# Kernel optimization log

Hardware: AMD Instinct MI355X
Metric: run time of the kernel (lower is better)

The kernel has to match this reference:

```python
import jax, jax.numpy as jnp
import numpy as np

N_NODES = 100000
NEG_SLOPE = 0.01


def setup_inputs() -> dict:
    key = jax.random.key(0)
    k1, k2, k3, k4 = jax.random.split(key, 4)
    E = 1600000
    x = jax.random.normal(k1, (N_NODES, 256), dtype=jnp.float32)
    edge_index = jax.random.randint(k2, (2, E), 0, N_NODES, dtype=jnp.int64)
    # Glorot-ish init for GCN linear weights
    W1 = jax.random.normal(k3, (256, 128), dtype=jnp.float32) / np.sqrt(256.0)
    b1 = jnp.zeros((128,), dtype=jnp.float32)
    W2 = jax.random.normal(k4, (128, 64), dtype=jnp.float32) / np.sqrt(128.0)
    b2 = jnp.zeros((64,), dtype=jnp.float32)
    return {"x": x, "edge_index": edge_index, "W1": W1, "b1": b1, "W2": W2, "b2": b2}


def _gcn_norm(edge_index, n_nodes):
    # Add self-loops (PyG GCNConv default), symmetric normalization.
    loops = jnp.arange(n_nodes, dtype=edge_index.dtype)
    src = jnp.concatenate([edge_index[0], loops])
    dst = jnp.concatenate([edge_index[1], loops])
    deg = jax.ops.segment_sum(jnp.ones_like(dst, dtype=jnp.float32), dst,
                              num_segments=n_nodes)
    dinv = jnp.where(deg > 0, 1.0 / jnp.sqrt(deg), 0.0)
    norm = dinv[src] * dinv[dst]  # [E + N]
    return src, dst, norm


def _gcn_conv(h, W, b, src, dst, norm, n_nodes):
    h = h @ W                              # [N, out] linear transform first
    msg = h[src] * norm[:, None]           # gather + edge weighting
    agg = jax.ops.segment_sum(msg, dst, num_segments=n_nodes)  # scatter-add
    return agg + b


def reference(x, edge_index, W1, b1, W2, b2):
    n = x.shape[0]
    src, dst, norm = _gcn_norm(edge_index, n)
    h = _gcn_conv(x, W1, b1, src, dst, norm, n)
    h = jnp.where(h >= 0, h, NEG_SLOPE * h)  # leaky_relu, slope 0.01
    return _gcn_conv(h, W2, b2, src, dst, norm, n)
```

## Files before the change

### kernel.cpp

```cpp
#include <hip/hip_runtime.h>
#include <hip/hip_bf16.h>
#include <stdint.h>

#define GPART 512
#define BSHIFT 9
#define BSIZE 512
#define MAXNB 512

typedef short short8 __attribute__((ext_vector_type(8)));
typedef float f32x4 __attribute__((ext_vector_type(4)));
union U4S8 { uint4 u; short8 s; };

static __device__ __forceinline__ float bflo(uint32_t h){ return __uint_as_float(h << 16); }
static __device__ __forceinline__ float bfhi(uint32_t h){ return __uint_as_float(h & 0xFFFF0000u); }
static __device__ __forceinline__ uint32_t f2bf_bits(float f){
  uint32_t u = __float_as_uint(f);
  return (u + 0x7FFFu + ((u >> 16) & 1u)) >> 16;
}
static __device__ __forceinline__ uint32_t pack2bf(float lo, float hi){
  return f2bf_bits(lo) | (f2bf_bits(hi) << 16);
}

__global__ __launch_bounds__(256) void k_hist(const int* __restrict__ dst, int E, int NB,
    int* __restrict__ gHist){
  __shared__ int lh[MAXNB];
  int blk = blockIdx.x;
  for (int i = threadIdx.x; i < NB; i += 256) lh[i] = 0;
  __syncthreads();
  int chunk = (E + GPART - 1) / GPART;
  int e0 = blk * chunk, e1 = min(E, e0 + chunk);
  for (int e = e0 + threadIdx.x; e < e1; e += 256)
    atomicAdd(&lh[dst[e] >> BSHIFT], 1);
  __syncthreads();
  for (int i = threadIdx.x; i < NB; i += 256) gHist[i * GPART + blk] = lh[i];
}

__global__ __launch_bounds__(64) void k_scanA(int* __restrict__ gHist,
    int* __restrict__ bucketTotal){
  int b = blockIdx.x;
  int lane = threadIdx.x;
  int carry = 0;
  #pragma unroll
  for (int r = 0; r < GPART/64; ++r){
    int v = gHist[b*GPART + r*64 + lane];
    int pref = v;
    #pragma unroll
    for (int off = 1; off < 64; off <<= 1){ int t = __shfl_up(pref, off); if (lane >= off) pref += t; }
    int tot = __shfl(pref, 63);
    gHist[b*GPART + r*64 + lane] = carry + pref - v;
    carry += tot;
  }
  if (lane == 0) bucketTotal[b] = carry;
}

__global__ __launch_bounds__(64) void k_scanB(const int* __restrict__ bucketTotal, int NB,
    int* __restrict__ bucketBase){
  int lane = threadIdx.x;
  int carry = 0;
  for (int r = 0; r*64 < NB; ++r){
    int idx = r*64 + lane;
    int v = (idx < NB) ? bucketTotal[idx] : 0;
    int pref = v;
    #pragma unroll
    for (int off = 1; off < 64; off <<= 1){ int t = __shfl_up(pref, off); if (lane >= off) pref += t; }
    int tot = __shfl(pref, 63);
    if (idx < NB) bucketBase[idx] = carry + pref - v;
    carry += tot;
  }
}

__global__ __launch_bounds__(256) void k_scatter(const int* __restrict__ src,
    const int* __restrict__ dst, int E, int NB,
    const int* __restrict__ gHist, const int* __restrict__ bucketBase,
    uint32_t* __restrict__ edgesP){
  __shared__ int lpos[MAXNB];
  int blk = blockIdx.x;
  for (int i = threadIdx.x; i < NB; i += 256) lpos[i] = 0;
  __syncthreads();
  int chunk = (E + GPART - 1) / GPART;
  int e0 = blk * chunk, e1 = min(E, e0 + chunk);
  for (int e = e0 + threadIdx.x; e < e1; e += 256){
    int s = src[e], d = dst[e];
    int b = d >> BSHIFT;
    int o = atomicAdd(&lpos[b], 1);
    int pos = bucketBase[b] + gHist[b*GPART + blk] + o;
    edgesP[pos] = (uint32_t)s | ((uint32_t)(d & (BSIZE-1)) << 23);
  }
}

__global__ __launch_bounds__(256) void k_csr_p1(const uint32_t* __restrict__ edgesP,
    const int* __restrict__ bucketBase, const int* __restrict__ bucketTotal,
    int n, int* __restrict__ start, int* __restrict__ cnt, float* __restrict__ dinv){
  __shared__ int cnt_l[BSIZE], start_l[BSIZE];
  int b = blockIdx.x;
  int base = bucketBase[b], total = bucketTotal[b];
  int d0 = b << BSHIFT;
  int tid = threadIdx.x;
  for (int i = tid; i < BSIZE; i += 256) cnt_l[i] = 0;
  __syncthreads();
  for (int i = tid; i < total; i += 256)
    atomicAdd(&cnt_l[edgesP[base + i] >> 23], 1);
  __syncthreads();
  if (tid < 64){
    int lane = tid, carry = 0;
    #pragma unroll
    for (int r = 0; r < BSIZE/64; ++r){
      int v = cnt_l[r*64 + lane];
      int pref = v;
      #pragma unroll
      for (int off = 1; off < 64; off <<= 1){ int t = __shfl_up(pref, off); if (lane >= off) pref += t; }
      int tot = __shfl(pref, 63);
      start_l[r*64 + lane] = carry + pref - v;
      carry += tot;
    }
  }
  __syncthreads();
  for (int i = tid; i < BSIZE; i += 256){
    int d = d0 + i;
    if (d < n){
      int c = cnt_l[i];
      cnt[d] = c;
      start[d] = base + start_l[i];
      dinv[d] = rsqrtf((float)(c + 1));
    }
  }
}

__global__ __launch_bounds__(256) void k_csr_p2(const uint32_t* __restrict__ edgesP,
    const int* __restrict__ bucketBase, const int* __restrict__ bucketTotal,
    const int* __restrict__ start, const float* __restrict__ dinv,
    int2* __restrict__ csr){
  __shared__ int fp[BSIZE];
  int b = blockIdx.x;
  int base = bucketBase[b], total = bucketTotal[b];
  int d0 = b << BSHIFT;
  int tid = threadIdx.x;
  for (int i = tid; i < BSIZE; i += 256) fp[i] = 0;
  __syncthreads();
  for (int i = tid; i < total; i += 256){
    uint32_t w = edgesP[base + i];
    int dl = (int)(w >> 23);
    int s = (int)(w & 0x7FFFFFu);
    int p = atomicAdd(&fp[dl], 1);
    float wt = dinv[s] * dinv[d0 + dl];
    csr[start[d0 + dl] + p] = make_int2(s, __float_as_int(wt));
  }
}

__global__ __launch_bounds__(256) void k_packW(const float* __restrict__ W,
    uint4* __restrict__ Wf, int K, int Nc){
  int s = blockIdx.x * 256 + threadIdx.x;
  int total = (K >> 5) * (Nc >> 4) * 64;
  if (s >= total) return;
  int lane = s & 63;
  int frag = s >> 6;
  int NT = Nc >> 4;
  int nt = frag % NT, ks = frag / NT;
  int col = nt*16 + (lane & 15);
  int k0  = ks*32 + (lane >> 4)*8;
  float v[8];
  #pragma unroll
  for (int e = 0; e < 8; ++e) v[e] = W[(size_t)(k0 + e)*Nc + col];
  uint4 u;
  u.x = pack2bf(v[0], v[1]); u.y = pack2bf(v[2], v[3]);
  u.z = pack2bf(v[4], v[5]); u.w = pack2bf(v[6], v[7]);
  Wf[s] = u;
}

__global__ __launch_bounds__(256) void k_gemm1_lds(const float* __restrict__ X,
    const uint4* __restrict__ W1f, unsigned short* __restrict__ H1, int n){
  __shared__ float xs[32][256];
  int tid = threadIdx.x;
  int wid = tid >> 6, lane = tid & 63;
  int row0 = blockIdx.x * 32;
  #pragma unroll
  for (int i = 0; i < 8; ++i){
    int r = wid*8 + i;
    int gr = min(row0 + r, n - 1);
    const float* gsrc = X + (size_t)gr*256 + 4*(lane ^ (r & 7));
    __builtin_amdgcn_global_load_lds(
        (const __attribute__((address_space(1))) unsigned int*)gsrc,
        (__attribute__((address_space(3))) unsigned int*)(&xs[r][0]),
        16, 0, 0);
  }
  __syncthreads();
  int mhalf = wid & 1, nh = wid >> 1;
  int rA = lane & 15, kg = lane >> 4;
  int lrow = mhalf*16 + rA;
  f32x4 acc[4];
  #pragma unroll
  for (int nt = 0; nt < 4; ++nt) acc[nt] = (f32x4){0.f, 0.f, 0.f, 0.f};
  #pragma unroll
  for (int ks = 0; ks < 8; ++ks){
    int g0 = ks*8 + kg*2;
    float4 f0 = *(const float4*)&xs[lrow][4*( g0      ^ (rA & 7))];
    float4 f1 = *(const float4*)&xs[lrow][4*((g0 + 1) ^ (rA & 7))];
    U4S8 a;
    a.u.x = pack2bf(f0.x, f0.y); a.u.y = pack2bf(f0.z, f0.w);
    a.u.z = pack2bf(f1.x, f1.y); a.u.w = pack2bf(f1.z, f1.w);
    #pragma unroll
    for (int nt = 0; nt < 4; ++nt){
      U4S8 b; b.u = W1f[(ks*8 + nh*4 + nt)*64 + lane];
      acc[nt] = __builtin_amdgcn_mfma_f32_16x16x32_bf16(a.s, b.s, acc[nt], 0, 0, 0);
    }
  }
  int rowbase = row0 + mhalf*16 + kg*4;
  #pragma unroll
  for (int r = 0; r < 4; ++r){
    int row = rowbase + r;
    if (row < n){
      #pragma unroll
      for (int nt = 0; nt < 4; ++nt)
        H1[(size_t)row*128 + (nh*4 + nt)*16 + rA] = (unsigned short)f2bf_bits(acc[nt][r]);
    }
  }
}

__global__ __launch_bounds__(256) void k_agg1(const uint4* __restrict__ H1,
    const int2* __restrict__ csr,
    const int* __restrict__ start, const int* __restrict__ cnt,
    const float* __restrict__ dinv, const float* __restrict__ b1,
    uint4* __restrict__ A1, int n){
  int w = (int)((blockIdx.x * blockDim.x + threadIdx.x) >> 6);
  int lane = threadIdx.x & 63;
  if (w >= n) return;
  int g = lane >> 4, li = lane & 15;
  float dw = dinv[w];
  float sw = (g == 0) ? dw * dw : 0.f;
  uint4 hs = H1[(size_t)w*16 + li];
  float acc[8];
  acc[0]=sw*bflo(hs.x); acc[1]=sw*bfhi(hs.x); acc[2]=sw*bflo(hs.y); acc[3]=sw*bfhi(hs.y);
  acc[4]=sw*bflo(hs.z); acc[5]=sw*bfhi(hs.z); acc[6]=sw*bflo(hs.w); acc[7]=sw*bfhi(hs.w);
  int e0 = start[w], deg = cnt[w];
  for (int base = 0; base < deg; base += 64){
    int nin = min(64, deg - base);
    int2 ew = (lane < nin) ? csr[e0 + base + lane] : make_int2(0, 0);
    for (int j = 0; j < nin; j += 8){
      int   sA = __shfl(ew.x, j + g);
      float wA = __uint_as_float((uint32_t)__shfl(ew.y, j + g));
      int   sB = __shfl(ew.x, j + 4 + g);
      float wB = __uint_as_float((uint32_t)__shfl(ew.y, j + 4 + g));
      uint4 hA = H1[(size_t)sA*16 + li];
      uint4 hB = H1[(size_t)sB*16 + li];
      acc[0]=fmaf(wA,bflo(hA.x),acc[0]); acc[1]=fmaf(wA,bfhi(hA.x),acc[1]);
      acc[2]=fmaf(wA,bflo(hA.y),acc[2]); acc[3]=fmaf(wA,bfhi(hA.y),acc[3]);
      acc[4]=fmaf(wA,bflo(hA.z),acc[4]); acc[5]=fmaf(wA,bfhi(hA.z),acc[5]);
      acc[6]=fmaf(wA,bflo(hA.w),acc[6]); acc[7]=fmaf(wA,bfhi(hA.w),acc[7]);
      acc[0]=fmaf(wB,bflo(hB.x),acc[0]); acc[1]=fmaf(wB,bfhi(hB.x),acc[1]);
      acc[2]=fmaf(wB,bflo(hB.y),acc[2]); acc[3]=fmaf(wB,bfhi(hB.y),acc[3]);
      acc[4]=fmaf(wB,bflo(hB.z),acc[4]); acc[5]=fmaf(wB,bfhi(hB.z),acc[5]);
      acc[6]=fmaf(wB,bflo(hB.w),acc[6]); acc[7]=fmaf(wB,bfhi(hB.w),acc[7]);
    }
  }
  #pragma unroll
  for (int e = 0; e < 8; ++e){
    acc[e] += __shfl_xor(acc[e], 16);
    acc[e] += __shfl_xor(acc[e], 32);
  }
  float4 bA = *(const float4*)&b1[li*8];
  float4 bB = *(const float4*)&b1[li*8 + 4];
  acc[0]+=bA.x; acc[1]+=bA.y; acc[2]+=bA.z; acc[3]+=bA.w;
  acc[4]+=bB.x; acc[5]+=bB.y; acc[6]+=bB.z; acc[7]+=bB.w;
  #pragma unroll
  for (int e = 0; e < 8; ++e) acc[e] = (acc[e] >= 0.f) ? acc[e] : 0.01f * acc[e];
  if (g == 0){
    uint4 o;
    o.x = pack2bf(acc[0], acc[1]); o.y = pack2bf(acc[2], acc[3]);
    o.z = pack2bf(acc[4], acc[5]); o.w = pack2bf(acc[6], acc[7]);
    A1[(size_t)w*16 + li] = o;
  }
}

__global__ __launch_bounds__(256) void k_gemm2_mfma(const uint4* __restrict__ A1,
    const uint4* __restrict__ W2f, unsigned short* __restrict__ H2, int n){
  int wv = (int)((blockIdx.x * 256u + threadIdx.x) >> 6);
  int lane = threadIdx.x & 63;
  int row0 = wv * 16;
  if (row0 >= n) return;
  int rA = lane & 15, kg = lane >> 4;
  f32x4 acc[4];
  #pragma unroll
  for (int nt = 0; nt < 4; ++nt) acc[nt] = (f32x4){0.f, 0.f, 0.f, 0.f};
  int r0 = min(row0 + rA, n - 1);
  const uint4* arow = A1 + (size_t)r0*16 + kg;
  uint4 u = arow[0];
  #pragma unroll
  for (int ks = 0; ks < 4; ++ks){
    U4S8 a; a.u = u;
    if (ks < 3) u = arow[(ks+1)*4];
    #pragma unroll
    for (int nt = 0; nt < 4; ++nt){
      U4S8 b; b.u = W2f[(ks*4 + nt)*64 + lane];
      acc[nt] = __builtin_amdgcn_mfma_f32_16x16x32_bf16(a.s, b.s, acc[nt], 0, 0, 0);
    }
  }
  #pragma unroll
  for (int r = 0; r < 4; ++r){
    int row = row0 + kg*4 + r;
    if (row < n){
      #pragma unroll
      for (int nt = 0; nt < 4; ++nt)
        H2[(size_t)row*64 + nt*16 + rA] = (unsigned short)f2bf_bits(acc[nt][r]);
    }
  }
}

__global__ __launch_bounds__(256) void k_agg2(const uint4* __restrict__ H2,
    const int2* __restrict__ csr,
    const int* __restrict__ start, const int* __restrict__ cnt,
    const float* __restrict__ dinv, const float* __restrict__ b2,
    float* __restrict__ out, int n){
  int w = (int)((blockIdx.x * blockDim.x + threadIdx.x) >> 6);
  int lane = threadIdx.x & 63;
  if (w >= n) return;
  int g = lane >> 3, li = lane & 7;
  float dw = dinv[w];
  float sw = (g == 0) ? dw * dw : 0.f;
  uint4 hs = H2[(size_t)w*8 + li];
  float acc[8];
  acc[0]=sw*bflo(hs.x); acc[1]=sw*bfhi(hs.x); acc[2]=sw*bflo(hs.y); acc[3]=sw*bfhi(hs.y);
  acc[4]=sw*bflo(hs.z); acc[5]=sw*bfhi(hs.z); acc[6]=sw*bflo(hs.w); acc[7]=sw*bfhi(hs.w);
  int e0 = start[w], deg = cnt[w];
  for (int base = 0; base < deg; base += 64){
    int nin = min(64, deg - base);
    int2 ew = (lane < nin) ? csr[e0 + base + lane] : make_int2(0, 0);
    for (int j = 0; j < nin; j += 16){
      int   sA = __shfl(ew.x, j + g);
      float wA = __uint_as_float((uint32_t)__shfl(ew.y, j + g));
      int   sB = __shfl(ew.x, j + 8 + g);
      float wB = __uint_as_float((uint32_t)__shfl(ew.y, j + 8 + g));
      uint4 hA = H2[(size_t)sA*8 + li];
      uint4 hB = H2[(size_t)sB*8 + li];
      acc[0]=fmaf(wA,bflo(hA.x),acc[0]); acc[1]=fmaf(wA,bfhi(hA.x),acc[1]);
      acc[2]=fmaf(wA,bflo(hA.y),acc[2]); acc[3]=fmaf(wA,bfhi(hA.y),acc[3]);
      acc[4]=fmaf(wA,bflo(hA.z),acc[4]); acc[5]=fmaf(wA,bfhi(hA.z),acc[5]);
      acc[6]=fmaf(wA,bflo(hA.w),acc[6]); acc[7]=fmaf(wA,bfhi(hA.w),acc[7]);
      acc[0]=fmaf(wB,bflo(hB.x),acc[0]); acc[1]=fmaf(wB,bfhi(hB.x),acc[1]);
      acc[2]=fmaf(wB,bflo(hB.y),acc[2]); acc[3]=fmaf(wB,bfhi(hB.y),acc[3]);
      acc[4]=fmaf(wB,bflo(hB.z),acc[4]); acc[5]=fmaf(wB,bfhi(hB.z),acc[5]);
      acc[6]=fmaf(wB,bflo(hB.w),acc[6]); acc[7]=fmaf(wB,bfhi(hB.w),acc[7]);
    }
  }
  #pragma unroll
  for (int e = 0; e < 8; ++e){
    acc[e] += __shfl_xor(acc[e], 8);
    acc[e] += __shfl_xor(acc[e], 16);
    acc[e] += __shfl_xor(acc[e], 32);
  }
  float4 bA = *(const float4*)&b2[li*8];
  float4 bB = *(const float4*)&b2[li*8 + 4];
  acc[0]+=bA.x; acc[1]+=bA.y; acc[2]+=bA.z; acc[3]+=bA.w;
  acc[4]+=bB.x; acc[5]+=bB.y; acc[6]+=bB.z; acc[7]+=bB.w;
  if (g == 0){
    float4 o0 = make_float4(acc[0], acc[1], acc[2], acc[3]);
    float4 o1 = make_float4(acc[4], acc[5], acc[6], acc[7]);
    *(float4*)&out[(size_t)w*64 + li*8]     = o0;
    *(float4*)&out[(size_t)w*64 + li*8 + 4] = o1;
  }
}

extern "C" void kernel_launch(void* const* d_in, const int* in_sizes, int n_in,
                              void* d_out, int out_size, void* d_ws, size_t ws_size,
                              hipStream_t stream){
  const float* x  = (const float*)d_in[0];
  const int*   ei = (const int*)d_in[1];
  const float* W1 = (const float*)d_in[2];
  const float* b1 = (const float*)d_in[3];
  const float* W2 = (const float*)d_in[4];
  const float* b2 = (const float*)d_in[5];
  float* out = (float*)d_out;

  int N = in_sizes[0] / 256;
  int E = in_sizes[1] / 2;
  int NB = (N + BSIZE - 1) >> BSHIFT;

  char* p = (char*)d_ws;
  uint32_t* H1   = (uint32_t*)p;  p += (size_t)N*64*4;
  uint32_t* A1   = (uint32_t*)p;  p += (size_t)N*64*4;
  uint32_t* H2   = (uint32_t*)p;  p += (size_t)N*32*4;
  uint32_t* edgesP=(uint32_t*)p;  p += (size_t)E*4;
  int2* csr      = (int2*)p;      p += (size_t)E*8;
  int* gHist     = (int*)p;       p += (size_t)NB*GPART*4;
  int* bucketTotal=(int*)p;       p += (size_t)((NB+63)&~63)*4;
  int* bucketBase= (int*)p;       p += (size_t)((NB+63)&~63)*4;
  uint4* W1f     = (uint4*)p;     p += 8*8*64*16;
  uint4* W2f     = (uint4*)p;     p += 4*4*64*16;
  int* start     = (int*)p;       p += (size_t)N*4;
  int* cnt       = (int*)p;       p += (size_t)N*4;
  float* dinv    = (float*)p;     p += (size_t)N*4;

  const int* srcIdx = ei;
  const int* dstIdx = ei + E;

  int nG1Blocks = (N + 31) / 32;
  int nW2 = (N + 15) / 16;
  int nG2Blocks = (nW2 + 3) / 4;
  int nNodeBlocks = (N + 3) / 4;

  k_packW<<<(8*8*64 + 255)/256, 256, 0, stream>>>(W1, W1f, 256, 128);
  k_packW<<<(4*4*64 + 255)/256, 256, 0, stream>>>(W2, W2f, 128, 64);
  k_hist<<<GPART, 256, 0, stream>>>(dstIdx, E, NB, gHist);
  k_scanA<<<NB, 64, 0, stream>>>(gHist, bucketTotal);
  k_scanB<<<1, 64, 0, stream>>>(bucketTotal, NB, bucketBase);
  k_scatter<<<GPART, 256, 0, stream>>>(srcIdx, dstIdx, E, NB, gHist, bucketBase, edgesP);
  k_csr_p1<<<NB, 256, 0, stream>>>(edgesP, bucketBase, bucketTotal, N, start, cnt, dinv);
  k_csr_p2<<<NB, 256, 0, stream>>>(edgesP, bucketBase, bucketTotal, start, dinv, csr);
  k_gemm1_lds<<<nG1Blocks, 256, 0, stream>>>(x, W1f, (unsigned short*)H1, N);
  k_agg1<<<nNodeBlocks, 256, 0, stream>>>((const uint4*)H1, csr, start, cnt, dinv, b1, (uint4*)A1, N);
  k_gemm2_mfma<<<nG2Blocks, 256, 0, stream>>>((const uint4*)A1, W2f, (unsigned short*)H2, N);
  k_agg2<<<nNodeBlocks, 256, 0, stream>>>((const uint4*)H2, csr, start, cnt, dinv, b2, out, N);
}
```

Baseline: 216.3 us.

## Split GEMM1 tiles across CSR-build kernels as extra blocks to overlap work

The standalone GEMM1 kernel is removed. Its 32-row tiles are distributed by fixed ratios across the histogram, scatter and two CSR-build kernels, which run as extra blocks alongside the graph-preprocessing blocks. This targets the idle CUs left by the small, latency-bound CSR kernels and drops one launch. In exchange every fused kernel reserves 32KB of shared memory, which can lower occupancy for the build blocks, and the split ratios are hand-tuned.

```diff
diff --git a/kernel.cpp b/kernel.cpp
--- a/kernel.cpp
+++ b/kernel.cpp
@@ -21,18 +21,75 @@
   return f2bf_bits(lo) | (f2bf_bits(hi) << 16);
 }
 
-__global__ __launch_bounds__(256) void k_hist(const int* __restrict__ dst, int E, int NB,
-    int* __restrict__ gHist){
-  __shared__ int lh[MAXNB];
+static __device__ __forceinline__ void gemm1_tile(const float* __restrict__ X,
+    const uint4* __restrict__ W1f, unsigned short* __restrict__ H1, int n,
+    int row0, char* smem, int tid){
+  float (*xs)[256] = (float (*)[256])smem;
+  int wid = tid >> 6, lane = tid & 63;
+  #pragma unroll
+  for (int i = 0; i < 8; ++i){
+    int r = wid*8 + i;
+    int gr = min(row0 + r, n - 1);
+    const float* gsrc = X + (size_t)gr*256 + 4*(lane ^ (r & 7));
+    __builtin_amdgcn_global_load_lds(
+        (const __attribute__((address_space(1))) unsigned int*)gsrc,
+        (__attribute__((address_space(3))) unsigned int*)(&xs[r][0]),
+        16, 0, 0);
+  }
+  __syncthreads();
+  int mhalf = wid & 1, nh = wid >> 1;
+  int rA = lane & 15, kg = lane >> 4;
+  int lrow = mhalf*16 + rA;
+  f32x4 acc[4];
+  #pragma unroll
+  for (int nt = 0; nt < 4; ++nt) acc[nt] = (f32x4){0.f, 0.f, 0.f, 0.f};
+  #pragma unroll
+  for (int ks = 0; ks < 8; ++ks){
+    int g0 = ks*8 + kg*2;
+    float4 f0 = *(const float4*)&xs[lrow][4*( g0      ^ (rA & 7))];
+    float4 f1 = *(const float4*)&xs[lrow][4*((g0 + 1) ^ (rA & 7))];
+    U4S8 a;
+    a.u.x = pack2bf(f0.x, f0.y); a.u.y = pack2bf(f0.z, f0.w);
+    a.u.z = pack2bf(f1.x, f1.y); a.u.w = pack2bf(f1.z, f1.w);
+    #pragma unroll
+    for (int nt = 0; nt < 4; ++nt){
+      U4S8 b; b.u = W1f[(ks*8 + nh*4 + nt)*64 + lane];
+      acc[nt] = __builtin_amdgcn_mfma_f32_16x16x32_bf16(a.s, b.s, acc[nt], 0, 0, 0);
+    }
+  }
+  int rowbase = row0 + mhalf*16 + kg*4;
+  #pragma unroll
+  for (int r = 0; r < 4; ++r){
+    int row = rowbase + r;
+    if (row < n){
+      #pragma unroll
+      for (int nt = 0; nt < 4; ++nt)
+        H1[(size_t)row*128 + (nh*4 + nt)*16 + rA] = (unsigned short)f2bf_bits(acc[nt][r]);
+    }
+  }
+}
+
+__global__ __launch_bounds__(256) void k_fat_hist(const int* __restrict__ dst, int E, int NB,
+    int* __restrict__ gHist,
+    const float* __restrict__ X, const uint4* __restrict__ W1f,
+    unsigned short* __restrict__ H1, int n, int g1base, int nbuild){
+  __shared__ __align__(16) char smem[32768];
+  int tid = threadIdx.x;
+  if ((int)blockIdx.x >= nbuild){
+    int row0 = (g1base + (int)blockIdx.x - nbuild) * 32;
+    gemm1_tile(X, W1f, H1, n, row0, smem, tid);
+    return;
+  }
+  int* lh = (int*)smem;
   int blk = blockIdx.x;
-  for (int i = threadIdx.x; i < NB; i += 256) lh[i] = 0;
+  for (int i = tid; i < NB; i += 256) lh[i] = 0;
   __syncthreads();
   int chunk = (E + GPART - 1) / GPART;
   int e0 = blk * chunk, e1 = min(E, e0 + chunk);
-  for (int e = e0 + threadIdx.x; e < e1; e += 256)
+  for (int e = e0 + tid; e < e1; e += 256)
     atomicAdd(&lh[dst[e] >> BSHIFT], 1);
   __syncthreads();
-  for (int i = threadIdx.x; i < NB; i += 256) gHist[i * GPART + blk] = lh[i];
+  for (int i = tid; i < NB; i += 256) gHist[i * GPART + blk] = lh[i];
 }
 
 __global__ __launch_bounds__(64) void k_scanA(int* __restrict__ gHist,
@@ -69,17 +126,26 @@
   }
 }
 
-__global__ __launch_bounds__(256) void k_scatter(const int* __restrict__ src,
+__global__ __launch_bounds__(256) void k_fat_scatter(const int* __restrict__ src,
     const int* __restrict__ dst, int E, int NB,
     const int* __restrict__ gHist, const int* __restrict__ bucketBase,
-    uint32_t* __restrict__ edgesP){
-  __shared__ int lpos[MAXNB];
+    uint32_t* __restrict__ edgesP,
+    const float* __restrict__ X, const uint4* __restrict__ W1f,
+    unsigned short* __restrict__ H1, int n, int g1base, int nbuild){
+  __shared__ __align__(16) char smem[32768];
+  int tid = threadIdx.x;
+  if ((int)blockIdx.x >= nbuild){
+    int row0 = (g1base + (int)blockIdx.x - nbuild) * 32;
+    gemm1_tile(X, W1f, H1, n, row0, smem, tid);
+    return;
+  }
+  int* lpos = (int*)smem;
   int blk = blockIdx.x;
-  for (int i = threadIdx.x; i < NB; i += 256) lpos[i] = 0;
+  for (int i = tid; i < NB; i += 256) lpos[i] = 0;
   __syncthreads();
   int chunk = (E + GPART - 1) / GPART;
   int e0 = blk * chunk, e1 = min(E, e0 + chunk);
-  for (int e = e0 + threadIdx.x; e < e1; e += 256){
+  for (int e = e0 + tid; e < e1; e += 256){
     int s = src[e], d = dst[e];
     int b = d >> BSHIFT;
     int o = atomicAdd(&lpos[b], 1);
@@ -88,14 +154,23 @@
   }
 }
 
-__global__ __launch_bounds__(256) void k_csr_p1(const uint32_t* __restrict__ edgesP,
+__global__ __launch_bounds__(256) void k_fat_p1(const uint32_t* __restrict__ edgesP,
     const int* __restrict__ bucketBase, const int* __restrict__ bucketTotal,
-    int n, int* __restrict__ start, int* __restrict__ cnt, float* __restrict__ dinv){
-  __shared__ int cnt_l[BSIZE], start_l[BSIZE];
+    int n, int* __restrict__ start, int* __restrict__ cnt, float* __restrict__ dinv,
+    const float* __restrict__ X, const uint4* __restrict__ W1f,
+    unsigned short* __restrict__ H1, int g1base, int nbuild){
+  __shared__ __align__(16) char smem[32768];
+  int tid = threadIdx.x;
+  if ((int)blockIdx.x >= nbuild){
+    int row0 = (g1base + (int)blockIdx.x - nbuild) * 32;
+    gemm1_tile(X, W1f, H1, n, row0, smem, tid);
+    return;
+  }
+  int* cnt_l   = (int*)smem;
+  int* start_l = (int*)(smem + BSIZE*4);
   int b = blockIdx.x;
   int base = bucketBase[b], total = bucketTotal[b];
   int d0 = b << BSHIFT;
-  int tid = threadIdx.x;
   for (int i = tid; i < BSIZE; i += 256) cnt_l[i] = 0;
   __syncthreads();
   for (int i = tid; i < total; i += 256)
@@ -126,15 +201,23 @@
   }
 }
 
-__global__ __launch_bounds__(256) void k_csr_p2(const uint32_t* __restrict__ edgesP,
+__global__ __launch_bounds__(256) void k_fat_p2(const uint32_t* __restrict__ edgesP,
     const int* __restrict__ bucketBase, const int* __restrict__ bucketTotal,
     const int* __restrict__ start, const float* __restrict__ dinv,
-    int2* __restrict__ csr){
-  __shared__ int fp[BSIZE];
+    int2* __restrict__ csr,
+    const float* __restrict__ X, const uint4* __restrict__ W1f,
+    unsigned short* __restrict__ H1, int n, int g1base, int nbuild){
+  __shared__ __align__(16) char smem[32768];
+  int tid = threadIdx.x;
+  if ((int)blockIdx.x >= nbuild){
+    int row0 = (g1base + (int)blockIdx.x - nbuild) * 32;
+    gemm1_tile(X, W1f, H1, n, row0, smem, tid);
+    return;
+  }
+  int* fp = (int*)smem;
   int b = blockIdx.x;
   int base = bucketBase[b], total = bucketTotal[b];
   int d0 = b << BSHIFT;
-  int tid = threadIdx.x;
   for (int i = tid; i < BSIZE; i += 256) fp[i] = 0;
   __syncthreads();
   for (int i = tid; i < total; i += 256){
@@ -165,55 +248,6 @@
   u.x = pack2bf(v[0], v[1]); u.y = pack2bf(v[2], v[3]);
   u.z = pack2bf(v[4], v[5]); u.w = pack2bf(v[6], v[7]);
   Wf[s] = u;
-}
-
-__global__ __launch_bounds__(256) void k_gemm1_lds(const float* __restrict__ X,
-    const uint4* __restrict__ W1f, unsigned short* __restrict__ H1, int n){
-  __shared__ float xs[32][256];
-  int tid = threadIdx.x;
-  int wid = tid >> 6, lane = tid & 63;
-  int row0 = blockIdx.x * 32;
-  #pragma unroll
-  for (int i = 0; i < 8; ++i){
-    int r = wid*8 + i;
-    int gr = min(row0 + r, n - 1);
-    const float* gsrc = X + (size_t)gr*256 + 4*(lane ^ (r & 7));
-    __builtin_amdgcn_global_load_lds(
-        (const __attribute__((address_space(1))) unsigned int*)gsrc,
-        (__attribute__((address_space(3))) unsigned int*)(&xs[r][0]),
-        16, 0, 0);
-  }
-  __syncthreads();
-  int mhalf = wid & 1, nh = wid >> 1;
-  int rA = lane & 15, kg = lane >> 4;
-  int lrow = mhalf*16 + rA;
-  f32x4 acc[4];
-  #pragma unroll
-  for (int nt = 0; nt < 4; ++nt) acc[nt] = (f32x4){0.f, 0.f, 0.f, 0.f};
-  #pragma unroll
-  for (int ks = 0; ks < 8; ++ks){
-    int g0 = ks*8 + kg*2;
-    float4 f0 = *(const float4*)&xs[lrow][4*( g0      ^ (rA & 7))];
-    float4 f1 = *(const float4*)&xs[lrow][4*((g0 + 1) ^ (rA & 7))];
-    U4S8 a;
-    a.u.x = pack2bf(f0.x, f0.y); a.u.y = pack2bf(f0.z, f0.w);
-    a.u.z = pack2bf(f1.x, f1.y); a.u.w = pack2bf(f1.z, f1.w);
-    #pragma unroll
-    for (int nt = 0; nt < 4; ++nt){
-      U4S8 b; b.u = W1f[(ks*8 + nh*4 + nt)*64 + lane];
-      acc[nt] = __builtin_amdgcn_mfma_f32_16x16x32_bf16(a.s, b.s, acc[nt], 0, 0, 0);
-    }
-  }
-  int rowbase = row0 + mhalf*16 + kg*4;
-  #pragma unroll
-  for (int r = 0; r < 4; ++r){
-    int row = rowbase + r;
-    if (row < n){
-      #pragma unroll
-      for (int nt = 0; nt < 4; ++nt)
-        H1[(size_t)row*128 + (nh*4 + nt)*16 + rA] = (unsigned short)f2bf_bits(acc[nt][r]);
-    }
-  }
 }
 
 __global__ __launch_bounds__(256) void k_agg1(const uint4* __restrict__ H1,
@@ -392,20 +426,30 @@
   const int* srcIdx = ei;
   const int* dstIdx = ei + E;
 
-  int nG1Blocks = (N + 31) / 32;
+  unsigned short* H1u = (unsigned short*)H1;
+
+  int G1 = (N + 31) / 32;
+  int sA = (int)((long)G1 * 20 / 100);
+  int sB = (int)((long)G1 * 33 / 100);
+  int sC = (int)((long)G1 * 18 / 100);
+  int sD = G1 - sA - sB - sC;
+
   int nW2 = (N + 15) / 16;
   int nG2Blocks = (nW2 + 3) / 4;
   int nNodeBlocks = (N + 3) / 4;
 
   k_packW<<<(8*8*64 + 255)/256, 256, 0, stream>>>(W1, W1f, 256, 128);
   k_packW<<<(4*4*64 + 255)/256, 256, 0, stream>>>(W2, W2f, 128, 64);
-  k_hist<<<GPART, 256, 0, stream>>>(dstIdx, E, NB, gHist);
+  k_fat_hist<<<GPART + sA, 256, 0, stream>>>(dstIdx, E, NB, gHist,
+      x, W1f, H1u, N, 0, GPART);
   k_scanA<<<NB, 64, 0, stream>>>(gHist, bucketTotal);
   k_scanB<<<1, 64, 0, stream>>>(bucketTotal, NB, bucketBase);
-  k_scatter<<<GPART, 256, 0, stream>>>(srcIdx, dstIdx, E, NB, gHist, bucketBase, edgesP);
-  k_csr_p1<<<NB, 256, 0, stream>>>(edgesP, bucketBase, bucketTotal, N, start, cnt, dinv);
-  k_csr_p2<<<NB, 256, 0, stream>>>(edgesP, bucketBase, bucketTotal, start, dinv, csr);
-  k_gemm1_lds<<<nG1Blocks, 256, 0, stream>>>(x, W1f, (unsigned short*)H1, N);
+  k_fat_scatter<<<GPART + sB, 256, 0, stream>>>(srcIdx, dstIdx, E, NB, gHist, bucketBase,
+      edgesP, x, W1f, H1u, N, sA, GPART);
+  k_fat_p1<<<NB + sC, 256, 0, stream>>>(edgesP, bucketBase, bucketTotal, N, start, cnt, dinv,
+      x, W1f, H1u, sA + sB, NB);
+  k_fat_p2<<<NB + sD, 256, 0, stream>>>(edgesP, bucketBase, bucketTotal, start, dinv, csr,
+      x, W1f, H1u, N, sA + sB + sC, NB);
   k_agg1<<<nNodeBlocks, 256, 0, stream>>>((const uint4*)H1, csr, start, cnt, dinv, b1, (uint4*)A1, N);
   k_gemm2_mfma<<<nG2Blocks, 256, 0, stream>>>((const uint4*)A1, W2f, (unsigned short*)H2, N);
   k_agg2<<<nNodeBlocks, 256, 0, stream>>>((const uint4*)H2, csr, start, cnt, dinv, b2, out, N);
```

Measured after the change: 212.4 us. Within noise of the previous version (-1.8%).
